# Optimization experiments

Measured on AMD Instinct MI355X. Metric: run time of the kernel, lower is better.

The kernel has to match this reference:

```python
import jax, jax.numpy as jnp
import numpy as np

D_MODEL = 1024
NHEAD = 16
DFF = 4096
B, S = 4, 1024
EPS = 1e-5  # torch LayerNorm default


def _layernorm(x, g, b):
    mu = jnp.mean(x, axis=-1, keepdims=True)
    var = jnp.mean((x - mu) ** 2, axis=-1, keepdims=True)
    return (x - mu) * jax.lax.rsqrt(var + EPS) * g + b


def setup_inputs() -> dict:
    key = jax.random.key(0)
    ks = jax.random.split(key, 12)
    sc = 0.02
    d, h, f = D_MODEL, NHEAD, DFF
    return {
        "src": jax.random.normal(ks[0], (B, S, d), dtype=jnp.float32),
        "w_in": jax.random.normal(ks[1], (3 * d, d), dtype=jnp.float32) * sc,  # packed q,k,v proj (torch in_proj_weight)
        "b_in": jnp.zeros((3 * d,), jnp.float32),
        "w_out": jax.random.normal(ks[2], (d, d), dtype=jnp.float32) * sc,
        "b_out": jnp.zeros((d,), jnp.float32),
        "w1": jax.random.normal(ks[3], (f, d), dtype=jnp.float32) * sc,
        "b1": jnp.zeros((f,), jnp.float32),
        "w2": jax.random.normal(ks[4], (d, f), dtype=jnp.float32) * sc,
        "b2": jnp.zeros((d,), jnp.float32),
        "g1": jnp.ones((d,), jnp.float32),
        "be1": jnp.zeros((d,), jnp.float32),
        "g2": jnp.ones((d,), jnp.float32),
        "be2": jnp.zeros((d,), jnp.float32),
    }


def reference(src, w_in, b_in, w_out, b_out, w1, b1, w2, b2, g1, be1, g2, be2):
    # dropout layers are identity in eval mode
    b, s, d = src.shape
    h = NHEAD
    dh = d // h
    # --- MHA, need_weights=True, average_attn_weights=False ---
    qkv = src @ w_in.T + b_in                      # [B,S,3D]
    q, k, v = jnp.split(qkv, 3, axis=-1)
    q = q.reshape(b, s, h, dh).transpose(0, 2, 1, 3) * (1.0 / np.sqrt(dh))
    k = k.reshape(b, s, h, dh).transpose(0, 2, 1, 3)
    v = v.reshape(b, s, h, dh).transpose(0, 2, 1, 3)
    scores = jnp.einsum("bhqd,bhkd->bhqk", q, k)   # [B,H,S,S]
    attn_weights = jax.nn.softmax(scores, axis=-1)  # per-head weights, materialized
    ctx = jnp.einsum("bhqk,bhkd->bhqd", attn_weights, v)
    ctx = ctx.transpose(0, 2, 1, 3).reshape(b, s, d)
    attn_out = ctx @ w_out.T + b_out
    # --- residual + LN1 ---
    x = _layernorm(src + attn_out, g1, be1)
    # --- FFN ---
    ff = jax.nn.relu(x @ w1.T + b1) @ w2.T + b2
    # --- residual + LN2 ---
    out = _layernorm(x + ff, g2, be2)
    return out, attn_weights
```

## Files before the change

### kernel.cpp

```cpp
#include <hip/hip_runtime.h>


#define DEVI __device__ __forceinline__

typedef __attribute__((ext_vector_type(4))) float f4;
typedef __attribute__((ext_vector_type(4))) float f32x4;
typedef __attribute__((ext_vector_type(8))) short s8;
typedef __attribute__((ext_vector_type(4))) unsigned short us4;
typedef unsigned short u16;

DEVI short bf16r(float f) {
  unsigned u = __builtin_bit_cast(unsigned, f);
  unsigned r = (u + 0x7fffu + ((u >> 16) & 1u)) >> 16;
  return (short)(unsigned short)r;
}
DEVI float bf2f(u16 h) {
  unsigned u = ((unsigned)h) << 16;
  return __builtin_bit_cast(float, u);
}
DEVI s8 cvt8(f4 a, f4 b) {
  s8 r;
  r[0] = bf16r(a.x); r[1] = bf16r(a.y); r[2] = bf16r(a.z); r[3] = bf16r(a.w);
  r[4] = bf16r(b.x); r[5] = bf16r(b.y); r[6] = bf16r(b.z); r[7] = bf16r(b.w);
  return r;
}

DEVI void gload16(const void* g, void* l) {
  __builtin_amdgcn_global_load_lds(
      (const __attribute__((address_space(1))) unsigned int*)g,
      (__attribute__((address_space(3))) unsigned int*)l, 16, 0, 0);
}

#define BAR()   __builtin_amdgcn_s_barrier()
#define LGKM0() do { asm volatile("s_waitcnt lgkmcnt(0)" ::: "memory"); \
                     __builtin_amdgcn_sched_barrier(0); } while (0)
#define VM4()   do { asm volatile("s_waitcnt vmcnt(4)" ::: "memory"); \
                     __builtin_amdgcn_sched_barrier(0); } while (0)

template<bool OUTBF16>
__global__ __launch_bounds__(512, 2)
void gemm256(const u16* __restrict__ A, long lda, long sA,
             const u16* __restrict__ B, long ldb, long sB,
             void* __restrict__ Cp, long ldc,
             long c0, long c1, long c2, long c3,
             const float* __restrict__ bias, int K,
             int qcols, float qscale, int do_relu)
{
  __shared__ __align__(128) char LDS[98304];

  const int tid = threadIdx.x, lane = tid & 63, w = tid >> 6;
  const int wr = w >> 2, wc = w & 3;
  const int z = blockIdx.z;
  const int row0 = blockIdx.y * 256, col0 = blockIdx.x * 256;

  const u16* Ag = A + (long)z * sA + (long)row0 * lda;
  const u16* Bg = B + (long)z * sB + (long)col0 * ldb;
  long coff = (z == 0) ? c0 : (z == 1) ? c1 : (z == 2) ? c2 : c3;

  const int NT = K >> 5;

  const int sr = (w << 4) + (lane >> 2);
  const int gsrc = (lane & 3) ^ ((sr >> 1) & 3);

  auto stageA = [&](int kt, int slot) {
#pragma unroll
    for (int h = 0; h < 2; ++h)
      gload16(Ag + (long)(h * 128 + sr) * lda + kt * 32 + gsrc * 8,
              LDS + slot * 16384 + h * 8192 + (w << 10));
  };
  auto stageB = [&](int kt, int slot) {
#pragma unroll
    for (int h = 0; h < 2; ++h)
      gload16(Bg + (long)(h * 128 + sr) * ldb + kt * 32 + gsrc * 8,
              LDS + 49152 + slot * 16384 + h * 8192 + (w << 10));
  };

  const int kg = lane >> 4, lr = lane & 15;
  auto rdA = [&](int buf, int fig, s8* aF) {
#pragma unroll
    for (int i = 0; i < 4; ++i) {
      int R = wr * 128 + (fig * 4 + i) * 16 + lr;
      aF[i] = *(const s8*)(LDS + buf * 16384 + R * 64 + ((kg ^ ((R >> 1) & 3)) << 4));
    }
  };
  auto rdB = [&](int buf, s8* bF) {
#pragma unroll
    for (int j = 0; j < 4; ++j) {
      int R = wc * 64 + j * 16 + lr;
      bF[j] = *(const s8*)(LDS + 49152 + buf * 16384 + R * 64 + ((kg ^ ((R >> 1) & 3)) << 4));
    }
  };

  f32x4 acc[8][4] = {};

  stageA(0, 0); stageB(0, 0);
  stageA(1, 1); stageB(1, 1);
  VM4();
  BAR();

  int buf = 0;
  for (int t = 0; t < NT; ++t) {
    int nbuf = buf + 2; if (nbuf >= 3) nbuf -= 3;
    int tc = (t + 2 < NT) ? t + 2 : NT - 1;
    s8 aF0[4], aF1[4], bF[4];

    stageA(tc, nbuf);
    stageB(tc, nbuf);
    rdB(buf, bF);
    rdA(buf, 0, aF0);
    rdA(buf, 1, aF1);
    BAR();
    LGKM0();
    __builtin_amdgcn_s_setprio(1);
#pragma unroll
    for (int i = 0; i < 4; ++i)
#pragma unroll
      for (int j = 0; j < 4; ++j)
        acc[i][j] = __builtin_amdgcn_mfma_f32_16x16x32_bf16(aF0[i], bF[j], acc[i][j], 0, 0, 0);
#pragma unroll
    for (int i = 0; i < 4; ++i)
#pragma unroll
      for (int j = 0; j < 4; ++j)
        acc[4 + i][j] = __builtin_amdgcn_mfma_f32_16x16x32_bf16(aF1[i], bF[j], acc[4 + i][j], 0, 0, 0);
    __builtin_amdgcn_s_setprio(0);
    VM4();
    BAR();
    buf = (buf == 2) ? 0 : buf + 1;
  }
  asm volatile("s_waitcnt vmcnt(0)" ::: "memory");

  float* Cf = (float*)Cp + coff;
  u16*   Cb = (u16*)Cp + coff;
#pragma unroll
  for (int fi = 0; fi < 8; ++fi) {
#pragma unroll
    for (int fj = 0; fj < 4; ++fj) {
      int rb = row0 + wr * 128 + fi * 16 + (lane >> 4) * 4;
      int c  = col0 + wc * 64 + fj * 16 + lr;
      float bv = bias ? bias[c] : 0.0f;
      float sc = (c < qcols) ? qscale : 1.0f;
#pragma unroll
      for (int q = 0; q < 4; ++q) {
        float v = (acc[fi][fj][q] + bv) * sc;
        if (do_relu) v = fmaxf(v, 0.0f);
        long idx = (long)(rb + q) * ldc + c;
        if constexpr (OUTBF16) Cb[idx] = (u16)bf16r(v);
        else                   Cf[idx] = v;
      }
    }
  }
}

__global__ __launch_bounds__(256)
void attn_fused(const u16* __restrict__ qkvb, const u16* __restrict__ vtb,
                float* __restrict__ attnW, u16* __restrict__ ctxb)
{
  __shared__ __align__(128) u16 Kt[128 * 64];
  __shared__ __align__(128) u16 Vt[64 * 128];
  __shared__ __align__(128) u16 Pt[4 * 32 * 128];

  int blk = blockIdx.x;
  int bh = blk >> 3, qt = blk & 7;
  int b = bh >> 4, h = bh & 15;
  int tid = threadIdx.x, lane = tid & 63, w = tid >> 6;

  const u16* Qg = qkvb + (long)b * 3145728 + (long)(qt * 128) * 3072 + h * 64;
#pragma unroll
  for (int c = 0; c < 4; ++c) {
    int seg = w * 4 + c;
    int r = seg * 8 + (lane >> 3);
    int g = (lane & 7) ^ (r & 7);
    gload16(Qg + (long)r * 3072 + g * 8, (char*)Kt + seg * 1024);
  }
  __syncthreads();
  s8 aq[2][2];
#pragma unroll
  for (int i = 0; i < 2; ++i)
#pragma unroll
    for (int kk = 0; kk < 2; ++kk) {
      int R = w * 32 + i * 16 + (lane & 15);
      int kgq = kk * 4 + (lane >> 4);
      aq[i][kk] = *(const s8*)((char*)Kt + R * 128 + ((kgq ^ (R & 7)) * 16));
    }

  const u16* Kbase = qkvb + (long)b * 3145728 + 1024 + h * 64;
  const u16* Vbase = vtb + (long)bh * 65536;

  float m[2][4], l[2][4];
#pragma unroll
  for (int i = 0; i < 2; ++i)
#pragma unroll
    for (int q = 0; q < 4; ++q) { m[i][q] = -1e30f; l[i][q] = 0.0f; }

  for (int kc = 0; kc < 8; ++kc) {
    __syncthreads();
#pragma unroll
    for (int c = 0; c < 4; ++c) {
      int seg = w * 4 + c;
      int r = seg * 8 + (lane >> 3);
      int g = (lane & 7) ^ (r & 7);
      gload16(Kbase + (long)(kc * 128 + r) * 3072 + g * 8, (char*)Kt + seg * 1024);
    }
    __syncthreads();

    f32x4 s[2][8] = {};
#pragma unroll
    for (int kk = 0; kk < 2; ++kk) {
      s8 bk[8];
      int kgq = kk * 4 + (lane >> 4);
#pragma unroll
      for (int j = 0; j < 8; ++j) {
        int R = j * 16 + (lane & 15);
        bk[j] = *(const s8*)((char*)Kt + R * 128 + ((kgq ^ (R & 7)) * 16));
      }
#pragma unroll
      for (int i = 0; i < 2; ++i)
#pragma unroll
        for (int j = 0; j < 8; ++j)
          s[i][j] = __builtin_amdgcn_mfma_f32_16x16x32_bf16(aq[i][kk], bk[j], s[i][j], 0, 0, 0);
    }

#pragma unroll
    for (int i = 0; i < 2; ++i)
#pragma unroll
      for (int q = 0; q < 4; ++q) {
        float mx = s[i][0][q];
#pragma unroll
        for (int j = 1; j < 8; ++j) mx = fmaxf(mx, s[i][j][q]);
        mx = fmaxf(mx, __shfl_xor(mx, 1));
        mx = fmaxf(mx, __shfl_xor(mx, 2));
        mx = fmaxf(mx, __shfl_xor(mx, 4));
        mx = fmaxf(mx, __shfl_xor(mx, 8));
        float mn = fmaxf(m[i][q], mx);
        float sum = 0.0f;
#pragma unroll
        for (int j = 0; j < 8; ++j) sum += __expf(s[i][j][q] - mn);
        sum += __shfl_xor(sum, 1);
        sum += __shfl_xor(sum, 2);
        sum += __shfl_xor(sum, 4);
        sum += __shfl_xor(sum, 8);
        l[i][q] = l[i][q] * __expf(m[i][q] - mn) + sum;
        m[i][q] = mn;
      }
  }

  float inv[2][4];
#pragma unroll
  for (int i = 0; i < 2; ++i)
#pragma unroll
    for (int q = 0; q < 4; ++q) inv[i][q] = 1.0f / l[i][q];

  f32x4 o_[2][4] = {};
  float* aw = attnW + (long)bh * 1048576 + (long)(qt * 128) * 1024;
  u16* Pw = Pt + w * 4096;

  for (int kc = 0; kc < 8; ++kc) {
    __syncthreads();
#pragma unroll
    for (int c = 0; c < 4; ++c) {
      int seg = w * 4 + c;
      int r = seg * 8 + (lane >> 3);
      int g = (lane & 7) ^ (r & 7);
      gload16(Kbase + (long)(kc * 128 + r) * 3072 + g * 8, (char*)Kt + seg * 1024);
    }
#pragma unroll
    for (int c = 0; c < 4; ++c) {
      int seg = w * 4 + c;
      int r = seg * 4 + (lane >> 4);
      int g = (lane & 15) ^ (r & 7);
      gload16(Vbase + (long)r * 1024 + kc * 128 + g * 8, (char*)Vt + seg * 1024);
    }
    __syncthreads();

    f32x4 s[2][8] = {};
#pragma unroll
    for (int kk = 0; kk < 2; ++kk) {
      s8 bk[8];
      int kgq = kk * 4 + (lane >> 4);
#pragma unroll
      for (int j = 0; j < 8; ++j) {
        int R = j * 16 + (lane & 15);
        bk[j] = *(const s8*)((char*)Kt + R * 128 + ((kgq ^ (R & 7)) * 16));
      }
#pragma unroll
      for (int i = 0; i < 2; ++i)
#pragma unroll
        for (int j = 0; j < 8; ++j)
          s[i][j] = __builtin_amdgcn_mfma_f32_16x16x32_bf16(aq[i][kk], bk[j], s[i][j], 0, 0, 0);
    }

#pragma unroll
    for (int i = 0; i < 2; ++i)
#pragma unroll
      for (int j = 0; j < 8; ++j)
#pragma unroll
        for (int q = 0; q < 4; ++q) {
          float p = __expf(s[i][j][q] - m[i][q]) * inv[i][q];
          int R = i * 16 + (lane >> 4) * 4 + q;
          int C = j * 16 + (lane & 15);
          aw[(long)(w * 32 + R) * 1024 + kc * 128 + C] = p;
          *(u16*)((char*)Pw + R * 256 + (((C >> 3) ^ (R & 7)) * 16) + (C & 7) * 2)
              = (u16)bf16r(p);
        }

#pragma unroll
    for (int kks = 0; kks < 4; ++kks) {
      int kgq = kks * 4 + (lane >> 4);
      s8 pa[2], bv[4];
#pragma unroll
      for (int i = 0; i < 2; ++i) {
        int R = i * 16 + (lane & 15);
        pa[i] = *(const s8*)((char*)Pw + R * 256 + ((kgq ^ (R & 7)) * 16));
      }
#pragma unroll
      for (int j = 0; j < 4; ++j) {
        int R = j * 16 + (lane & 15);
        bv[j] = *(const s8*)((char*)Vt + R * 256 + ((kgq ^ (R & 7)) * 16));
      }
#pragma unroll
      for (int i = 0; i < 2; ++i)
#pragma unroll
        for (int j = 0; j < 4; ++j)
          o_[i][j] = __builtin_amdgcn_mfma_f32_16x16x32_bf16(pa[i], bv[j], o_[i][j], 0, 0, 0);
    }
  }

#pragma unroll
  for (int i = 0; i < 2; ++i)
#pragma unroll
    for (int j = 0; j < 4; ++j)
#pragma unroll
      for (int q = 0; q < 4; ++q) {
        int R = w * 32 + i * 16 + (lane >> 4) * 4 + q;
        int col = h * 64 + j * 16 + (lane & 15);
        ctxb[(long)(b * 1024 + qt * 128 + R) * 1024 + col] = (u16)bf16r(o_[i][j][q]);
      }
}

DEVI float blockSum(float v, float* sh) {
#pragma unroll
  for (int o = 32; o > 0; o >>= 1) v += __shfl_xor(v, o);
  int w = threadIdx.x >> 6;
  __syncthreads();
  if ((threadIdx.x & 63) == 0) sh[w] = v;
  __syncthreads();
  return (sh[0] + sh[1]) + (sh[2] + sh[3]);
}

template<bool RBF16>
__global__ __launch_bounds__(256)
void ln_combine4(const float* __restrict__ P0, const float* __restrict__ P1,
                 const float* __restrict__ P2, const float* __restrict__ P3,
                 const void* __restrict__ resid, const float* __restrict__ bias,
                 const float* __restrict__ g, const float* __restrict__ be,
                 float* __restrict__ outf, u16* __restrict__ outb)
{
  __shared__ float sh[4];
  long row = blockIdx.x;
  int t = threadIdx.x;
  long off = row * 1024 + t * 4;
  f4 v = *(const f4*)(P0 + off);
  v += *(const f4*)(P1 + off);
  v += *(const f4*)(P2 + off);
  v += *(const f4*)(P3 + off);
  if constexpr (RBF16) {
    us4 rp = *(const us4*)((const u16*)resid + off);
    v.x += bf2f(rp.x); v.y += bf2f(rp.y); v.z += bf2f(rp.z); v.w += bf2f(rp.w);
  } else {
    v += *(const f4*)((const float*)resid + off);
  }
  v += *(const f4*)(bias + t * 4);
  float s = (v.x + v.y) + (v.z + v.w);
  s = blockSum(s, sh);
  float mu = s * (1.0f / 1024.0f);
  f4 d = v - mu;
  float s2 = (d.x * d.x + d.y * d.y) + (d.z * d.z + d.w * d.w);
  s2 = blockSum(s2, sh);
  float rs = rsqrtf(s2 * (1.0f / 1024.0f) + 1e-5f);
  f4 gg = *(const f4*)(g + t * 4);
  f4 bb = *(const f4*)(be + t * 4);
  f4 o = d * rs * gg + bb;
  if (outf) *(f4*)(outf + off) = o;
  if (outb) {
    us4 ob;
    ob.x = (u16)bf16r(o.x); ob.y = (u16)bf16r(o.y);
    ob.z = (u16)bf16r(o.z); ob.w = (u16)bf16r(o.w);
    *(us4*)(outb + off) = ob;
  }
}

__global__ __launch_bounds__(256)
void cvt_all(const float* __restrict__ s0, const float* __restrict__ s1,
             const float* __restrict__ s2, const float* __restrict__ s3,
             const float* __restrict__ s4,
             u16* __restrict__ d0, u16* __restrict__ d1, u16* __restrict__ d2,
             u16* __restrict__ d3, u16* __restrict__ d4)
{
  int bi = blockIdx.x;
  const float* s; u16* d; int base;
  if      (bi < 2048) { s = s0; d = d0; base = bi; }
  else if (bi < 3584) { s = s1; d = d1; base = bi - 2048; }
  else if (bi < 4096) { s = s2; d = d2; base = bi - 3584; }
  else if (bi < 6144) { s = s3; d = d3; base = bi - 4096; }
  else                { s = s4; d = d4; base = bi - 6144; }
  long i = ((long)base * 256 + threadIdx.x) * 8;
  f4 a = *(const f4*)(s + i);
  f4 b = *(const f4*)(s + i + 4);
  *(s8*)(d + i) = cvt8(a, b);
}

__global__ __launch_bounds__(256)
void transpose_v(const u16* __restrict__ qkv, u16* __restrict__ vt) {
  __shared__ u16 tile[64][72];
  int blk = blockIdx.x, bh = blk >> 4, st = blk & 15;
  int b = bh >> 4, h = bh & 15, s0 = st * 64;
  const u16* gq = qkv + (long)b * 1024 * 3072 + 2048 + (long)h * 64;
  int t = threadIdx.x;
  int sl = t >> 4, dq = (t & 15) * 4;
#pragma unroll
  for (int it = 0; it < 4; ++it) {
    int s = it * 16 + sl;
    us4 v = *(const us4*)(gq + (long)(s0 + s) * 3072 + dq);
    tile[dq + 0][s] = v.x; tile[dq + 1][s] = v.y;
    tile[dq + 2][s] = v.z; tile[dq + 3][s] = v.w;
  }
  __syncthreads();
  u16* o = vt + (long)bh * 65536 + s0;
  int dl = t >> 4, sq = (t & 15) * 4;
#pragma unroll
  for (int it = 0; it < 4; ++it) {
    int d = it * 16 + dl;
    us4 v;
    v.x = tile[d][sq + 0]; v.y = tile[d][sq + 1];
    v.z = tile[d][sq + 2]; v.w = tile[d][sq + 3];
    *(us4*)(o + (long)d * 1024 + sq) = v;
  }
}

extern "C" void kernel_launch(void* const* d_in, const int* in_sizes, int n_in,
                              void* d_out, int out_size, void* d_ws, size_t ws_size,
                              hipStream_t stream)
{
  (void)in_sizes; (void)n_in; (void)out_size; (void)ws_size;
  const float* src   = (const float*)d_in[0];
  const float* w_in  = (const float*)d_in[1];
  const float* b_in  = (const float*)d_in[2];
  const float* w_out = (const float*)d_in[3];
  const float* b_out = (const float*)d_in[4];
  const float* w1    = (const float*)d_in[5];
  const float* b1    = (const float*)d_in[6];
  const float* w2    = (const float*)d_in[7];
  const float* b2    = (const float*)d_in[8];
  const float* g1    = (const float*)d_in[9];
  const float* be1   = (const float*)d_in[10];
  const float* g2    = (const float*)d_in[11];
  const float* be2   = (const float*)d_in[12];

  float* out   = (float*)d_out;
  float* attnW = out + (long)4 * 1024 * 1024;

  char* ws = (char*)d_ws;
  u16*   qkvb   = (u16*)(ws);
  u16*   vtb    = (u16*)(ws + 25165824);
  u16*   srcb   = (u16*)(ws + 33554432);
  u16*   ctxb   = (u16*)(ws + 41943040);
  u16*   xb     = (u16*)(ws + 50331648);
  u16*   w_in_b = (u16*)(ws + 58720256);
  u16*   w_outb = (u16*)(ws + 65011712);
  u16*   w1b    = (u16*)(ws + 67108864);
  u16*   w2b    = (u16*)(ws + 75497472);
  u16*   h1b    = (u16*)(ws);
  const long Q0 = 0,        Q1 = 4194304,  Q2 = 20971520, Q3 = 25165824;
  const long R0 = 8388608,  R1 = 14680064, R2 = 20971520, R3 = 25165824;
  float* wsf = (float*)ws;

  cvt_all<<<dim3(8192), 256, 0, stream>>>(src, w_in, w_out, w1, w2,
                                          srcb, w_in_b, w_outb, w1b, w2b);

  gemm256<true><<<dim3(12, 16, 1), 512, 0, stream>>>(
      srcb, 1024, 0, w_in_b, 1024, 0, qkvb, 3072, 0, 0, 0, 0,
      b_in, 1024, 1024, 0.125f, 0);

  transpose_v<<<dim3(1024), 256, 0, stream>>>(qkvb, vtb);

  attn_fused<<<dim3(512), 256, 0, stream>>>(qkvb, vtb, attnW, ctxb);

  gemm256<false><<<dim3(4, 16, 4), 512, 0, stream>>>(
      ctxb, 1024, 256, w_outb, 1024, 256, wsf, 1024, Q0, Q1, Q2, Q3,
      nullptr, 256, 0, 1.0f, 0);

  ln_combine4<false><<<dim3(4096), 256, 0, stream>>>(
      wsf + Q0, wsf + Q1, wsf + Q2, wsf + Q3, src, b_out, g1, be1, nullptr, xb);

  gemm256<true><<<dim3(16, 16, 1), 512, 0, stream>>>(
      xb, 1024, 0, w1b, 1024, 0, h1b, 4096, 0, 0, 0, 0,
      b1, 1024, 0, 1.0f, 1);

  gemm256<false><<<dim3(4, 16, 4), 512, 0, stream>>>(
      h1b, 4096, 1024, w2b, 4096, 1024, wsf, 1024, R0, R1, R2, R3,
      nullptr, 1024, 0, 1.0f, 0);

  ln_combine4<true><<<dim3(4096), 256, 0, stream>>>(
      wsf + R0, wsf + R1, wsf + R2, wsf + R3, xb, b2, g2, be2, out, nullptr);
}
```

Baseline: 325.6 us.

## Replace split-K GEMMs with 128-tile GEMMs fusing bias and residual

```diff
diff --git a/kernel.cpp b/kernel.cpp
--- a/kernel.cpp
+++ b/kernel.cpp
@@ -37,25 +37,112 @@
 #define VM4()   do { asm volatile("s_waitcnt vmcnt(4)" ::: "memory"); \
                      __builtin_amdgcn_sched_barrier(0); } while (0)
 
-template<bool OUTBF16>
-__global__ __launch_bounds__(512, 2)
-void gemm256(const u16* __restrict__ A, long lda, long sA,
-             const u16* __restrict__ B, long ldb, long sB,
-             void* __restrict__ Cp, long ldc,
-             long c0, long c1, long c2, long c3,
-             const float* __restrict__ bias, int K,
+DEVI void xcd_remap(int& bx, int& by) {
+  int nbx = gridDim.x, nby = gridDim.y;
+  int hw = blockIdx.y * nbx + blockIdx.x;
+  int qch = (nbx * nby) >> 3;
+  int lid = (hw & 7) * qch + (hw >> 3);
+  bx = lid % nbx; by = lid / nbx;
+}
+
+template<int RES>
+__global__ __launch_bounds__(256)
+void gemm128(const u16* __restrict__ A, long lda,
+             const u16* __restrict__ B, long ldb,
+             u16* __restrict__ C, long ldc,
+             const float* __restrict__ bias,
+             const void* __restrict__ resid, long ldr, int K,
              int qcols, float qscale, int do_relu)
 {
+  __shared__ __align__(128) short As[128 * 64];
+  __shared__ __align__(128) short Bs[128 * 64];
+
+  int bx, by; xcd_remap(bx, by);
+  int row0 = by * 128, col0 = bx * 128;
+  int tid = threadIdx.x, lane = tid & 63, w = tid >> 6;
+  int wr = w >> 1, wc = w & 1;
+
+  const u16* Ab = A + (long)row0 * lda;
+  const u16* Bb = B + (long)col0 * ldb;
+
+  f32x4 acc[4][4] = {};
+
+  for (int k0 = 0; k0 < K; k0 += 64) {
+    if (k0) __syncthreads();
+#pragma unroll
+    for (int c = 0; c < 4; ++c) {
+      int seg = w * 4 + c;
+      int r = seg * 8 + (lane >> 3);
+      int g = (lane & 7) ^ (r & 7);
+      gload16(Ab + (long)r * lda + k0 + g * 8, (char*)As + seg * 1024);
+    }
+#pragma unroll
+    for (int c = 0; c < 4; ++c) {
+      int seg = w * 4 + c;
+      int r = seg * 8 + (lane >> 3);
+      int g = (lane & 7) ^ (r & 7);
+      gload16(Bb + (long)r * ldb + k0 + g * 8, (char*)Bs + seg * 1024);
+    }
+    __syncthreads();
+
+#pragma unroll
+    for (int kk = 0; kk < 2; ++kk) {
+      s8 af[4], bf[4];
+      int lr = lane & 15, kg = kk * 4 + (lane >> 4);
+#pragma unroll
+      for (int i = 0; i < 4; ++i) {
+        int R = wr * 64 + i * 16 + lr;
+        af[i] = *(const s8*)((char*)As + R * 128 + ((kg ^ (R & 7)) * 16));
+      }
+#pragma unroll
+      for (int j = 0; j < 4; ++j) {
+        int R = wc * 64 + j * 16 + lr;
+        bf[j] = *(const s8*)((char*)Bs + R * 128 + ((kg ^ (R & 7)) * 16));
+      }
+#pragma unroll
+      for (int i = 0; i < 4; ++i)
+#pragma unroll
+        for (int j = 0; j < 4; ++j)
+          acc[i][j] = __builtin_amdgcn_mfma_f32_16x16x32_bf16(af[i], bf[j], acc[i][j], 0, 0, 0);
+    }
+  }
+
+#pragma unroll
+  for (int i = 0; i < 4; ++i) {
+#pragma unroll
+    for (int j = 0; j < 4; ++j) {
+      int rb = row0 + wr * 64 + i * 16 + (lane >> 4) * 4;
+      int c  = col0 + wc * 64 + j * 16 + (lane & 15);
+      float bv = bias ? bias[c] : 0.0f;
+      float sc = (c < qcols) ? qscale : 1.0f;
+#pragma unroll
+      for (int q = 0; q < 4; ++q) {
+        float v = (acc[i][j][q] + bv) * sc;
+        if (do_relu) v = fmaxf(v, 0.0f);
+        long rr = rb + q;
+        if constexpr (RES == 1) v += ((const float*)resid)[rr * ldr + c];
+        if constexpr (RES == 2) v += bf2f(((const u16*)resid)[rr * ldr + c]);
+        C[rr * ldc + c] = (u16)bf16r(v);
+      }
+    }
+  }
+}
+
+__global__ __launch_bounds__(512, 2)
+void gemm256(const u16* __restrict__ A, long lda,
+             const u16* __restrict__ B, long ldb,
+             u16* __restrict__ C, long ldc,
+             const float* __restrict__ bias, int K, int do_relu)
+{
   __shared__ __align__(128) char LDS[98304];
 
   const int tid = threadIdx.x, lane = tid & 63, w = tid >> 6;
   const int wr = w >> 2, wc = w & 3;
-  const int z = blockIdx.z;
-  const int row0 = blockIdx.y * 256, col0 = blockIdx.x * 256;
-
-  const u16* Ag = A + (long)z * sA + (long)row0 * lda;
-  const u16* Bg = B + (long)z * sB + (long)col0 * ldb;
-  long coff = (z == 0) ? c0 : (z == 1) ? c1 : (z == 2) ? c2 : c3;
+  int bx, by; xcd_remap(bx, by);
+  const int row0 = by * 256, col0 = bx * 256;
+
+  const u16* Ag = A + (long)row0 * lda;
+  const u16* Bg = B + (long)col0 * ldb;
 
   const int NT = K >> 5;
 
@@ -129,8 +216,6 @@
   }
   asm volatile("s_waitcnt vmcnt(0)" ::: "memory");
 
-  float* Cf = (float*)Cp + coff;
-  u16*   Cb = (u16*)Cp + coff;
 #pragma unroll
   for (int fi = 0; fi < 8; ++fi) {
 #pragma unroll
@@ -138,14 +223,11 @@
       int rb = row0 + wr * 128 + fi * 16 + (lane >> 4) * 4;
       int c  = col0 + wc * 64 + fj * 16 + lr;
       float bv = bias ? bias[c] : 0.0f;
-      float sc = (c < qcols) ? qscale : 1.0f;
 #pragma unroll
       for (int q = 0; q < 4; ++q) {
-        float v = (acc[fi][fj][q] + bv) * sc;
+        float v = acc[fi][fj][q] + bv;
         if (do_relu) v = fmaxf(v, 0.0f);
-        long idx = (long)(rb + q) * ldc + c;
-        if constexpr (OUTBF16) Cb[idx] = (u16)bf16r(v);
-        else                   Cf[idx] = v;
+        C[(long)(rb + q) * ldc + c] = (u16)bf16r(v);
       }
     }
   }
@@ -347,29 +429,18 @@
   return (sh[0] + sh[1]) + (sh[2] + sh[3]);
 }
 
-template<bool RBF16>
 __global__ __launch_bounds__(256)
-void ln_combine4(const float* __restrict__ P0, const float* __restrict__ P1,
-                 const float* __restrict__ P2, const float* __restrict__ P3,
-                 const void* __restrict__ resid, const float* __restrict__ bias,
-                 const float* __restrict__ g, const float* __restrict__ be,
-                 float* __restrict__ outf, u16* __restrict__ outb)
+void ln_rows_b(const u16* __restrict__ in, const float* __restrict__ g,
+               const float* __restrict__ be,
+               float* __restrict__ outf, u16* __restrict__ outb)
 {
   __shared__ float sh[4];
   long row = blockIdx.x;
   int t = threadIdx.x;
   long off = row * 1024 + t * 4;
-  f4 v = *(const f4*)(P0 + off);
-  v += *(const f4*)(P1 + off);
-  v += *(const f4*)(P2 + off);
-  v += *(const f4*)(P3 + off);
-  if constexpr (RBF16) {
-    us4 rp = *(const us4*)((const u16*)resid + off);
-    v.x += bf2f(rp.x); v.y += bf2f(rp.y); v.z += bf2f(rp.z); v.w += bf2f(rp.w);
-  } else {
-    v += *(const f4*)((const float*)resid + off);
-  }
-  v += *(const f4*)(bias + t * 4);
+  us4 rp = *(const us4*)(in + off);
+  f4 v;
+  v.x = bf2f(rp.x); v.y = bf2f(rp.y); v.z = bf2f(rp.z); v.w = bf2f(rp.w);
   float s = (v.x + v.y) + (v.z + v.w);
   s = blockSum(s, sh);
   float mu = s * (1.0f / 1024.0f);
@@ -469,37 +540,33 @@
   u16*   w_outb = (u16*)(ws + 65011712);
   u16*   w1b    = (u16*)(ws + 67108864);
   u16*   w2b    = (u16*)(ws + 75497472);
+  u16*   xsumb  = (u16*)(ws + 83886080);
+  u16*   ffsumb = (u16*)(ws + 92274688);
   u16*   h1b    = (u16*)(ws);
-  const long Q0 = 0,        Q1 = 4194304,  Q2 = 20971520, Q3 = 25165824;
-  const long R0 = 8388608,  R1 = 14680064, R2 = 20971520, R3 = 25165824;
-  float* wsf = (float*)ws;
 
   cvt_all<<<dim3(8192), 256, 0, stream>>>(src, w_in, w_out, w1, w2,
                                           srcb, w_in_b, w_outb, w1b, w2b);
 
-  gemm256<true><<<dim3(12, 16, 1), 512, 0, stream>>>(
-      srcb, 1024, 0, w_in_b, 1024, 0, qkvb, 3072, 0, 0, 0, 0,
-      b_in, 1024, 1024, 0.125f, 0);
+  gemm128<0><<<dim3(24, 32), 256, 0, stream>>>(
+      srcb, 1024, w_in_b, 1024, qkvb, 3072,
+      b_in, nullptr, 0, 1024, 1024, 0.125f, 0);
 
   transpose_v<<<dim3(1024), 256, 0, stream>>>(qkvb, vtb);
 
   attn_fused<<<dim3(512), 256, 0, stream>>>(qkvb, vtb, attnW, ctxb);
 
-  gemm256<false><<<dim3(4, 16, 4), 512, 0, stream>>>(
-      ctxb, 1024, 256, w_outb, 1024, 256, wsf, 1024, Q0, Q1, Q2, Q3,
-      nullptr, 256, 0, 1.0f, 0);
-
-  ln_combine4<false><<<dim3(4096), 256, 0, stream>>>(
-      wsf + Q0, wsf + Q1, wsf + Q2, wsf + Q3, src, b_out, g1, be1, nullptr, xb);
-
-  gemm256<true><<<dim3(16, 16, 1), 512, 0, stream>>>(
-      xb, 1024, 0, w1b, 1024, 0, h1b, 4096, 0, 0, 0, 0,
-      b1, 1024, 0, 1.0f, 1);
-
-  gemm256<false><<<dim3(4, 16, 4), 512, 0, stream>>>(
-      h1b, 4096, 1024, w2b, 4096, 1024, wsf, 1024, R0, R1, R2, R3,
-      nullptr, 1024, 0, 1.0f, 0);
-
-  ln_combine4<true><<<dim3(4096), 256, 0, stream>>>(
-      wsf + R0, wsf + R1, wsf + R2, wsf + R3, xb, b2, g2, be2, out, nullptr);
-}
+  gemm128<1><<<dim3(8, 32), 256, 0, stream>>>(
+      ctxb, 1024, w_outb, 1024, xsumb, 1024,
+      b_out, src, 1024, 1024, 0, 1.0f, 0);
+
+  ln_rows_b<<<dim3(4096), 256, 0, stream>>>(xsumb, g1, be1, nullptr, xb);
+
+  gemm256<<<dim3(16, 16), 512, 0, stream>>>(
+      xb, 1024, w1b, 1024, h1b, 4096, b1, 1024, 1);
+
+  gemm128<2><<<dim3(8, 32), 256, 0, stream>>>(
+      h1b, 4096, w2b, 4096, ffsumb, 1024,
+      b2, xb, 1024, 4096, 0, 1.0f, 0);
+
+  ln_rows_b<<<dim3(4096), 256, 0, stream>>>(ffsumb, g2, be2, out, nullptr);
+}
```

New measurement: 330.1 us. About the same (+1.4%).
